# Performance work log

Hardware: AMD Instinct MI355X
Metric: run time of the kernel (lower is better)

Reference implementation:

```python
import jax, jax.numpy as jnp
import numpy as np
import math

IN_FEATURES = 512
RFF_FEATURES = 2048
OUT_FEATURES = 1000
N = 8192
RIDGE_PENALTY = 1.0
MEAN_FIELD_FACTOR = 25.0
RFF_SCALAR = math.sqrt(RFF_FEATURES / 2)  # 32.0


def _random_ortho(key, n, m):
    q, _ = jnp.linalg.qr(jax.random.normal(key, (n, m), dtype=jnp.float32))
    return q


def setup_inputs() -> dict:
    key = jax.random.key(0)
    k_d, k_w, k_norm, k_b, k_lw, k_lb, k_cov = jax.random.split(key, 7)
    D = jax.random.normal(k_d, (N, IN_FEATURES), dtype=jnp.float32)
    # RFF weight: concat of random orthonormal blocks (rff_features > in_features)
    ws = []
    dim_left = RFF_FEATURES
    kk = k_w
    while dim_left > IN_FEATURES:
        kk, sub = jax.random.split(kk)
        ws.append(_random_ortho(sub, IN_FEATURES, IN_FEATURES))
        dim_left -= IN_FEATURES
    kk, sub = jax.random.split(kk)
    ws.append(_random_ortho(sub, IN_FEATURES, dim_left))
    W = jnp.concatenate(ws, axis=1)  # [in, rff]
    feature_norm = jax.random.normal(k_norm, W.shape, dtype=jnp.float32) ** 2
    W = W * jnp.sqrt(feature_norm.sum(0))
    b = jax.random.uniform(k_b, (RFF_FEATURES,), dtype=jnp.float32) * (2.0 * math.pi)
    # logit head (nn.Linear): weight [out, rff], bias [out]
    bound = 1.0 / math.sqrt(RFF_FEATURES)
    logit_w = jax.random.uniform(k_lw, (OUT_FEATURES, RFF_FEATURES), dtype=jnp.float32,
                                 minval=-bound, maxval=bound)
    logit_b = jax.random.uniform(k_lb, (OUT_FEATURES,), dtype=jnp.float32,
                                 minval=-bound, maxval=bound)
    # positive-definite covariance buffer (stand-in for inverted precision)
    A = jax.random.normal(k_cov, (RFF_FEATURES, RFF_FEATURES), dtype=jnp.float32) * 0.01
    covariance = A @ A.T + jnp.eye(RFF_FEATURES, dtype=jnp.float32)
    return {"D": D, "W": W, "b": b, "logit_w": logit_w, "logit_b": logit_b,
            "covariance": covariance}


def reference(D, W, b, logit_w, logit_b, covariance):
    # RFF feature map: cos(D @ W + b) / rff_scalar  -> [N, rff]
    Phi = jnp.cos(D @ W + b) / RFF_SCALAR
    # linear head -> [N, out]
    pred = Phi @ logit_w.T + logit_b
    # diag(Phi @ cov @ Phi.T) * ridge computed row-wise in O(N*r^2)
    diag_cov = jnp.sum((Phi @ covariance) * Phi, axis=-1) * RIDGE_PENALTY  # [N]
    logits_scale = jnp.sqrt(1.0 + diag_cov * MEAN_FIELD_FACTOR)
    return pred / logits_scale[:, None]
```

## Files before the change

kernel.cpp:

```cpp
#include <hip/hip_runtime.h>
#include <hip/hip_fp8.h>
#include <math.h>

#define N_ROWS 8192
#define IN_F   512
#define RFF    2048
#define OUT_F  1000
#define OUT_PAD 1024
#define INV_RFF_SCALAR 0.03125f
#define MEAN_FIELD 25.0f

typedef __attribute__((ext_vector_type(8))) short short8;
typedef __attribute__((ext_vector_type(4))) float f32x4;

__device__ __forceinline__ unsigned short f32_to_bf16(float f) {
    unsigned u = __float_as_uint(f);
    unsigned r = 0x7FFFu + ((u >> 16) & 1u);
    return (unsigned short)((u + r) >> 16);
}
__device__ __forceinline__ float bf16_to_f32(unsigned short h) {
    return __uint_as_float(((unsigned)h) << 16);
}
__device__ __forceinline__ unsigned char f32_to_fp8(float x) {
    __hip_fp8_e4m3 q(x);
    return (unsigned char)q.__x;
}

__device__ __forceinline__ const uint4* gsrc(const unsigned short* X, int ldx,
                                             int r0, int k0, int q) {
    int rt = q >> 6, L = q & 63;
    int r = r0 + rt * 16 + (L & 15);
    int k = k0 + ((L >> 4) << 3);
    return (const uint4*)(X + (size_t)r * ldx + k);
}

__device__ __forceinline__ void stage_tile(const unsigned short* __restrict__ X, int ldx,
                                           int r0, int k0, unsigned short* lds,
                                           int w, int lane) {
    #pragma unroll
    for (int half = 0; half < 2; ++half) {
        int qb = half * 256 + w * 64;
        const uint4* g = gsrc(X, ldx, r0, k0, qb + lane);
        __builtin_amdgcn_global_load_lds(
            (const __attribute__((address_space(1))) void*)g,
            (__attribute__((address_space(3))) void*)(lds + qb * 8),
            16, 0, 0);
    }
}

__device__ __forceinline__ void stage_tile8(const unsigned char* __restrict__ X, int ldb,
                                            int r0, int k0b, unsigned char* lds,
                                            int w, int lane) {
    #pragma unroll
    for (int half = 0; half < 2; ++half) {
        int qb = half * 256 + w * 64;
        int q = qb + lane;
        int rt = q >> 6, L = q & 63;
        int row = r0 + rt * 16 + (L & 15);
        int kb = k0b + ((L >> 4) << 4);
        const void* g = X + (size_t)row * ldb + kb;
        __builtin_amdgcn_global_load_lds(
            (const __attribute__((address_space(1))) void*)g,
            (__attribute__((address_space(3))) void*)(lds + qb * 16),
            16, 0, 0);
    }
}

__global__ __launch_bounds__(256) void conv_split_kernel(
    const float* __restrict__ X, unsigned short* __restrict__ H,
    unsigned short* __restrict__ L, int n4)
{
    int i = blockIdx.x * 256 + threadIdx.x;
    if (i >= n4) return;
    float4 v = ((const float4*)X)[i];
    ushort4 h, l;
    h.x = f32_to_bf16(v.x); l.x = f32_to_bf16(v.x - bf16_to_f32(h.x));
    h.y = f32_to_bf16(v.y); l.y = f32_to_bf16(v.y - bf16_to_f32(h.y));
    h.z = f32_to_bf16(v.z); l.z = f32_to_bf16(v.z - bf16_to_f32(h.z));
    h.w = f32_to_bf16(v.w); l.w = f32_to_bf16(v.w - bf16_to_f32(h.w));
    ((ushort4*)H)[i] = h;
    ((ushort4*)L)[i] = l;
}

__global__ __launch_bounds__(256) void conv_covu8_kernel(
    const float* __restrict__ X, unsigned char* __restrict__ O)
{
    int i = blockIdx.x * 256 + threadIdx.x;
    int base = i * 4;
    int row = base >> 11;
    int col = base & 2047;
    int bn = row >> 7, bk = col >> 7;
    float w = (bk < bn) ? 16.0f : (bk == bn ? 8.0f : 0.0f);
    float4 v = ((const float4*)X)[i];
    float w0 = (col + 0 == row) ? 0.0f : w;
    float w1 = (col + 1 == row) ? 0.0f : w;
    float w2 = (col + 2 == row) ? 0.0f : w;
    float w3 = (col + 3 == row) ? 0.0f : w;
    uchar4 o;
    o.x = f32_to_fp8(v.x * w0); o.y = f32_to_fp8(v.y * w1);
    o.z = f32_to_fp8(v.z * w2); o.w = f32_to_fp8(v.w * w3);
    ((uchar4*)O)[i] = o;
}

__global__ __launch_bounds__(256) void conv_covd_kernel(
    const float* __restrict__ X, float* __restrict__ Cd)
{
    int i = blockIdx.x * 256 + threadIdx.x;
    if (i < RFF) Cd[i] = X[(size_t)i * RFF + i];
}

__global__ __launch_bounds__(256) void conv_phi8_kernel(
    const unsigned short* __restrict__ Phi16, unsigned char* __restrict__ Phi8)
{
    int i = blockIdx.x * 256 + threadIdx.x;
    ushort4 v = ((const ushort4*)Phi16)[i];
    uchar4 o;
    o.x = f32_to_fp8(bf16_to_f32(v.x) * 32.0f);
    o.y = f32_to_fp8(bf16_to_f32(v.y) * 32.0f);
    o.z = f32_to_fp8(bf16_to_f32(v.z) * 32.0f);
    o.w = f32_to_fp8(bf16_to_f32(v.w) * 32.0f);
    ((uchar4*)Phi8)[i] = o;
}

__global__ __launch_bounds__(256) void conv_lw_kernel(
    const float* __restrict__ Lw, unsigned short* __restrict__ O)
{
    int i = blockIdx.x * 256 + threadIdx.x;
    int base = i * 4;
    int row = base >> 11;
    ushort4 o;
    if (row < OUT_F) {
        float4 v = ((const float4*)Lw)[i];
        o.x = f32_to_bf16(v.x); o.y = f32_to_bf16(v.y);
        o.z = f32_to_bf16(v.z); o.w = f32_to_bf16(v.w);
    } else {
        o.x = o.y = o.z = o.w = 0;
    }
    ((ushort4*)O)[i] = o;
}

__global__ __launch_bounds__(256) void conv_wt_kernel(
    const float* __restrict__ W, unsigned short* __restrict__ TH,
    unsigned short* __restrict__ TL)
{
    __shared__ float tile[64][65];
    const int tid = threadIdx.x;
    const int n0 = blockIdx.x * 64;
    const int k0 = blockIdx.y * 64;
    #pragma unroll
    for (int i = 0; i < 16; ++i) {
        int e = i * 256 + tid;
        int r = e >> 6, c = e & 63;
        tile[r][c] = W[(size_t)(k0 + r) * RFF + n0 + c];
    }
    __syncthreads();
    #pragma unroll
    for (int i = 0; i < 16; ++i) {
        int e = i * 256 + tid;
        int r = e >> 6, c = e & 63;
        float v = tile[c][r];
        unsigned short h = f32_to_bf16(v);
        unsigned short l = f32_to_bf16(v - bf16_to_f32(h));
        TH[(size_t)(n0 + r) * IN_F + k0 + c] = h;
        TL[(size_t)(n0 + r) * IN_F + k0 + c] = l;
    }
}

__global__ __launch_bounds__(256) void phi_mfma_kernel(
    const unsigned short* __restrict__ Dh, const unsigned short* __restrict__ Dl,
    const unsigned short* __restrict__ Wth, const unsigned short* __restrict__ Wtl,
    const float* __restrict__ bias, unsigned short* __restrict__ Phi)
{
    __shared__ unsigned short ldsAh[4096], ldsAl[4096], ldsBh[4096], ldsBl[4096];
    const int tid = threadIdx.x;
    const int w = tid >> 6, lane = tid & 63;
    const int wm = w >> 1, wn = w & 1;
    const int r0 = blockIdx.y * 128;
    const int c0 = blockIdx.x * 128;

    f32x4 acc[4][4];
    #pragma unroll
    for (int i = 0; i < 4; ++i)
        #pragma unroll
        for (int j = 0; j < 4; ++j)
            acc[i][j] = (f32x4)(0.0f);

    for (int k0 = 0; k0 < IN_F; k0 += 32) {
        __syncthreads();
        stage_tile(Dh,  IN_F, r0, k0, ldsAh, w, lane);
        stage_tile(Dl,  IN_F, r0, k0, ldsAl, w, lane);
        stage_tile(Wth, IN_F, c0, k0, ldsBh, w, lane);
        stage_tile(Wtl, IN_F, c0, k0, ldsBl, w, lane);
        __syncthreads();

        short8 fah[4], fal[4], fbh[4], fbl[4];
        #pragma unroll
        for (int t = 0; t < 4; ++t) {
            fah[t] = *(const short8*)(ldsAh + ((wm * 4 + t) * 64 + lane) * 8);
            fal[t] = *(const short8*)(ldsAl + ((wm * 4 + t) * 64 + lane) * 8);
            fbh[t] = *(const short8*)(ldsBh + ((wn * 4 + t) * 64 + lane) * 8);
            fbl[t] = *(const short8*)(ldsBl + ((wn * 4 + t) * 64 + lane) * 8);
        }
        #pragma unroll
        for (int mt = 0; mt < 4; ++mt)
            #pragma unroll
            for (int nt = 0; nt < 4; ++nt) {
                acc[mt][nt] = __builtin_amdgcn_mfma_f32_16x16x32_bf16(
                    fah[mt], fbh[nt], acc[mt][nt], 0, 0, 0);
                acc[mt][nt] = __builtin_amdgcn_mfma_f32_16x16x32_bf16(
                    fah[mt], fbl[nt], acc[mt][nt], 0, 0, 0);
                acc[mt][nt] = __builtin_amdgcn_mfma_f32_16x16x32_bf16(
                    fal[mt], fbh[nt], acc[mt][nt], 0, 0, 0);
            }
    }

    const int quad = lane >> 4, ln = lane & 15;
    #pragma unroll
    for (int mt = 0; mt < 4; ++mt)
        #pragma unroll
        for (int nt = 0; nt < 4; ++nt) {
            int col = c0 + wn * 64 + nt * 16 + ln;
            float bv = bias[col];
            #pragma unroll
            for (int reg = 0; reg < 4; ++reg) {
                int row = r0 + wm * 64 + mt * 16 + quad * 4 + reg;
                float z = acc[mt][nt][reg] + bv;
                float p = __cosf(z) * INV_RFF_SCALAR;
                Phi[(size_t)row * RFF + col] = f32_to_bf16(p);
            }
        }
}

__global__ __launch_bounds__(256) void fused_dp_kernel(
    const unsigned short* __restrict__ Phi16, const unsigned char* __restrict__ Phi8,
    const unsigned char* __restrict__ CovU8, const float* __restrict__ Cd,
    const unsigned short* __restrict__ Lw, const float* __restrict__ Lb,
    float* __restrict__ diag, float* __restrict__ out)
{
    __shared__ __align__(16) unsigned char smem[16384];
    const int tid = threadIdx.x;
    const int w = tid >> 6, lane = tid & 63;
    const int wm = w >> 1, wn = w & 1;
    const int quad = lane >> 4, ln = lane & 15;
    const int b = blockIdx.x;

    f32x4 acc[4][4];
    #pragma unroll
    for (int i = 0; i < 4; ++i)
        #pragma unroll
        for (int j = 0; j < 4; ++j)
            acc[i][j] = (f32x4)(0.0f);

    if (b % 3 != 2) {
        const int d = (b / 3) * 2 + (b % 3);
        const int J = 15 - (d >> 6);
        const int r0 = (d & 63) * 128;
        const int c0 = J * 128;
        const int kmaxb = (J + 1) * 128;
        unsigned char* ldsA8 = smem;
        unsigned char* ldsB8 = smem + 8192;

        for (int k0b = 0; k0b < kmaxb; k0b += 64) {
            __syncthreads();
            stage_tile8(Phi8,  RFF, r0, k0b, ldsA8, w, lane);
            stage_tile8(CovU8, RFF, c0, k0b, ldsB8, w, lane);
            __syncthreads();

            #pragma unroll
            for (int s = 0; s < 2; ++s) {
                const int ccol = s * 2 + (quad >> 1);
                const int off8 = (quad & 1) << 3;
                long fa[4], fb[4];
                #pragma unroll
                for (int t = 0; t < 4; ++t) {
                    fa[t] = *(const long*)(ldsA8 + (((wm * 4 + t) * 64 + ccol * 16 + ln) << 4) + off8);
                    fb[t] = *(const long*)(ldsB8 + (((wn * 4 + t) * 64 + ccol * 16 + ln) << 4) + off8);
                }
                #pragma unroll
                for (int mt = 0; mt < 4; ++mt)
                    #pragma unroll
                    for (int nt = 0; nt < 4; ++nt)
                        acc[mt][nt] = __builtin_amdgcn_mfma_f32_16x16x32_fp8_fp8(
                            fa[mt], fb[nt], acc[mt][nt], 0, 0, 0);
            }
        }

        float cd[4];
        #pragma unroll
        for (int nt = 0; nt < 4; ++nt)
            cd[nt] = 256.0f * Cd[c0 + wn * 64 + nt * 16 + ln];
        #pragma unroll
        for (int mt = 0; mt < 4; ++mt) {
            float psum[4] = {0.f, 0.f, 0.f, 0.f};
            #pragma unroll
            for (int nt = 0; nt < 4; ++nt) {
                int col = c0 + wn * 64 + nt * 16 + ln;
                #pragma unroll
                for (int reg = 0; reg < 4; ++reg) {
                    int row = r0 + wm * 64 + mt * 16 + quad * 4 + reg;
                    float pv = bf16_to_f32(Phi16[(size_t)row * RFF + col]);
                    psum[reg] = fmaf(fmaf(cd[nt], pv, acc[mt][nt][reg]), pv, psum[reg]);
                }
            }
            #pragma unroll
            for (int off = 1; off < 16; off <<= 1)
                #pragma unroll
                for (int reg = 0; reg < 4; ++reg)
                    psum[reg] += __shfl_xor(psum[reg], off, 16);
            if (ln == 0) {
                #pragma unroll
                for (int reg = 0; reg < 4; ++reg) {
                    int row = r0 + wm * 64 + mt * 16 + quad * 4 + reg;
                    atomicAdd(&diag[row], psum[reg] * (1.0f / 256.0f));
                }
            }
        }
    } else {
        const int p = b / 3;
        const int r0 = (p >> 3) * 128;
        const int c0 = (p & 7) * 128;
        unsigned short* ldsA = (unsigned short*)smem;
        unsigned short* ldsB = (unsigned short*)(smem + 8192);

        for (int k0 = 0; k0 < RFF; k0 += 32) {
            __syncthreads();
            stage_tile(Phi16, RFF, r0, k0, ldsA, w, lane);
            stage_tile(Lw,    RFF, c0, k0, ldsB, w, lane);
            __syncthreads();

            short8 fa[4], fb[4];
            #pragma unroll
            for (int t = 0; t < 4; ++t) {
                fa[t] = *(const short8*)(ldsA + ((wm * 4 + t) * 64 + lane) * 8);
                fb[t] = *(const short8*)(ldsB + ((wn * 4 + t) * 64 + lane) * 8);
            }
            #pragma unroll
            for (int mt = 0; mt < 4; ++mt)
                #pragma unroll
                for (int nt = 0; nt < 4; ++nt)
                    acc[mt][nt] = __builtin_amdgcn_mfma_f32_16x16x32_bf16(
                        fa[mt], fb[nt], acc[mt][nt], 0, 0, 0);
        }

        #pragma unroll
        for (int mt = 0; mt < 4; ++mt)
            #pragma unroll
            for (int nt = 0; nt < 4; ++nt) {
                int col = c0 + wn * 64 + nt * 16 + ln;
                if (col < OUT_F) {
                    float bv = Lb[col];
                    #pragma unroll
                    for (int reg = 0; reg < 4; ++reg) {
                        int row = r0 + wm * 64 + mt * 16 + quad * 4 + reg;
                        out[(size_t)row * OUT_F + col] = acc[mt][nt][reg] + bv;
                    }
                }
            }
    }
}

__global__ __launch_bounds__(256) void scale_kernel(
    float* __restrict__ out, const float* __restrict__ diag)
{
    const int row = blockIdx.x;
    const int t = threadIdx.x;
    float s = 1.0f / sqrtf(1.0f + MEAN_FIELD * diag[row]);
    if (t < 250) {
        float4* p = (float4*)(out + (size_t)row * OUT_F);
        float4 v = p[t];
        v.x *= s; v.y *= s; v.z *= s; v.w *= s;
        p[t] = v;
    }
}

extern "C" void kernel_launch(void* const* d_in, const int* in_sizes, int n_in,
                              void* d_out, int out_size, void* d_ws, size_t ws_size,
                              hipStream_t stream) {
    const float* D    = (const float*)d_in[0];
    const float* W    = (const float*)d_in[1];
    const float* bias = (const float*)d_in[2];
    const float* Lw   = (const float*)d_in[3];
    const float* Lb   = (const float*)d_in[4];
    const float* cov  = (const float*)d_in[5];
    float* out = (float*)d_out;

    char* p = (char*)d_ws;
    unsigned short* Phi16 = (unsigned short*)p;  p += (size_t)N_ROWS * RFF * 2;
    unsigned char*  Phi8  = (unsigned char*)p;
    unsigned short* Dh    = (unsigned short*)p;  p += (size_t)N_ROWS * IN_F * 2;
    unsigned short* Dl    = (unsigned short*)p;  p += (size_t)N_ROWS * IN_F * 2;
    unsigned short* Wth   = (unsigned short*)p;  p += (size_t)RFF * IN_F * 2;
    unsigned short* Wtl   = (unsigned short*)p;  p += (size_t)RFF * IN_F * 2;
    unsigned short* Lw16  = (unsigned short*)p;  p += (size_t)OUT_PAD * RFF * 2;
    unsigned char*  CovU8 = (unsigned char*)p;
    float*          Cd    = (float*)(p + (size_t)RFF * RFF);
    p += (size_t)RFF * RFF * 2;
    float* diag           = (float*)p;

    hipMemsetAsync(diag, 0, N_ROWS * sizeof(float), stream);

    dim3 blk(256);
    conv_split_kernel<<<dim3((N_ROWS * IN_F / 4 + 255) / 256), blk, 0, stream>>>(D, Dh, Dl, N_ROWS * IN_F / 4);
    conv_wt_kernel<<<dim3(RFF / 64, IN_F / 64), blk, 0, stream>>>(W, Wth, Wtl);
    conv_lw_kernel<<<dim3(OUT_PAD * RFF / 4 / 256), blk, 0, stream>>>(Lw, Lw16);
    conv_covu8_kernel<<<dim3(RFF * RFF / 4 / 256), blk, 0, stream>>>(cov, CovU8);
    conv_covd_kernel<<<dim3(RFF / 256), blk, 0, stream>>>(cov, Cd);

    phi_mfma_kernel<<<dim3(RFF / 128, N_ROWS / 128), blk, 0, stream>>>(Dh, Dl, Wth, Wtl, bias, Phi16);
    conv_phi8_kernel<<<dim3(N_ROWS * RFF / 4 / 256), blk, 0, stream>>>(Phi16, Phi8);

    fused_dp_kernel<<<dim3(1536), blk, 0, stream>>>(Phi16, Phi8, CovU8, Cd, Lw16, Lb, diag, out);
    scale_kernel<<<dim3(N_ROWS), blk, 0, stream>>>(out, diag);
}
```

Baseline: 365.3 us.

## Split fused diag/pred kernel, permute fp8 layouts, fold scaling into pred epilogue

```diff
diff --git a/kernel.cpp b/kernel.cpp
--- a/kernel.cpp
+++ b/kernel.cpp
@@ -12,6 +12,7 @@
 
 typedef __attribute__((ext_vector_type(8))) short short8;
 typedef __attribute__((ext_vector_type(4))) float f32x4;
+typedef __attribute__((ext_vector_type(2))) long long2v;
 
 __device__ __forceinline__ unsigned short f32_to_bf16(float f) {
     unsigned u = __float_as_uint(f);
@@ -24,6 +25,10 @@
 __device__ __forceinline__ unsigned char f32_to_fp8(float x) {
     __hip_fp8_e4m3 q(x);
     return (unsigned char)q.__x;
+}
+
+__device__ __forceinline__ int perm64(int k) {
+    return (k & ~63) | (((k >> 3) & 3) << 4) | (((k >> 5) & 1) << 3) | (k & 7);
 }
 
 __device__ __forceinline__ const uint4* gsrc(const unsigned short* X, int ldx,
@@ -33,7 +38,6 @@
     int k = k0 + ((L >> 4) << 3);
     return (const uint4*)(X + (size_t)r * ldx + k);
 }
-
 __device__ __forceinline__ void stage_tile(const unsigned short* __restrict__ X, int ldx,
                                            int r0, int k0, unsigned short* lds,
                                            int w, int lane) {
@@ -48,17 +52,31 @@
     }
 }
 
-__device__ __forceinline__ void stage_tile8(const unsigned char* __restrict__ X, int ldb,
+__device__ __forceinline__ void stage_tile64(const unsigned short* __restrict__ X,
+                                             int r0, int k0, unsigned char* lds,
+                                             int w, int lane) {
+    #pragma unroll
+    for (int h = 0; h < 4; ++h) {
+        int qb = h * 256 + w * 64;
+        int q = qb + lane;
+        int rt = q >> 7, c = (q >> 4) & 7, r = q & 15;
+        const void* g = X + (size_t)(r0 + rt * 16 + r) * RFF + k0 + c * 8;
+        __builtin_amdgcn_global_load_lds(
+            (const __attribute__((address_space(1))) void*)g,
+            (__attribute__((address_space(3))) void*)(lds + qb * 16),
+            16, 0, 0);
+    }
+}
+
+__device__ __forceinline__ void stage_tile8(const unsigned char* __restrict__ X,
                                             int r0, int k0b, unsigned char* lds,
                                             int w, int lane) {
     #pragma unroll
-    for (int half = 0; half < 2; ++half) {
-        int qb = half * 256 + w * 64;
+    for (int h = 0; h < 4; ++h) {
+        int qb = h * 256 + w * 64;
         int q = qb + lane;
-        int rt = q >> 6, L = q & 63;
-        int row = r0 + rt * 16 + (L & 15);
-        int kb = k0b + ((L >> 4) << 4);
-        const void* g = X + (size_t)row * ldb + kb;
+        int rt = q >> 7, c = (q >> 4) & 7, r = q & 15;
+        const void* g = X + (size_t)(r0 + rt * 16 + r) * RFF + k0b + c * 16;
         __builtin_amdgcn_global_load_lds(
             (const __attribute__((address_space(1))) void*)g,
             (__attribute__((address_space(3))) void*)(lds + qb * 16),
@@ -99,7 +117,7 @@
     uchar4 o;
     o.x = f32_to_fp8(v.x * w0); o.y = f32_to_fp8(v.y * w1);
     o.z = f32_to_fp8(v.z * w2); o.w = f32_to_fp8(v.w * w3);
-    ((uchar4*)O)[i] = o;
+    *(uchar4*)(O + (size_t)row * RFF + perm64(col)) = o;
 }
 
 __global__ __launch_bounds__(256) void conv_covd_kernel(
@@ -113,13 +131,16 @@
     const unsigned short* __restrict__ Phi16, unsigned char* __restrict__ Phi8)
 {
     int i = blockIdx.x * 256 + threadIdx.x;
+    int base = i * 4;
+    int row = base >> 11;
+    int col = base & 2047;
     ushort4 v = ((const ushort4*)Phi16)[i];
     uchar4 o;
     o.x = f32_to_fp8(bf16_to_f32(v.x) * 32.0f);
     o.y = f32_to_fp8(bf16_to_f32(v.y) * 32.0f);
     o.z = f32_to_fp8(bf16_to_f32(v.z) * 32.0f);
     o.w = f32_to_fp8(bf16_to_f32(v.w) * 32.0f);
-    ((uchar4*)Phi8)[i] = o;
+    *(uchar4*)(Phi8 + (size_t)row * RFF + perm64(col)) = o;
 }
 
 __global__ __launch_bounds__(256) void conv_lw_kernel(
@@ -231,18 +252,21 @@
         }
 }
 
-__global__ __launch_bounds__(256) void fused_dp_kernel(
-    const unsigned short* __restrict__ Phi16, const unsigned char* __restrict__ Phi8,
-    const unsigned char* __restrict__ CovU8, const float* __restrict__ Cd,
-    const unsigned short* __restrict__ Lw, const float* __restrict__ Lb,
-    float* __restrict__ diag, float* __restrict__ out)
-{
-    __shared__ __align__(16) unsigned char smem[16384];
+__global__ __launch_bounds__(256) void diag8_kernel(
+    const unsigned char* __restrict__ Phi8, const unsigned char* __restrict__ CovU8,
+    const unsigned short* __restrict__ Phi16, const float* __restrict__ Cd,
+    float* __restrict__ diag)
+{
+    __shared__ __align__(16) unsigned char ldsA[16384];
+    __shared__ __align__(16) unsigned char ldsB[16384];
     const int tid = threadIdx.x;
     const int w = tid >> 6, lane = tid & 63;
     const int wm = w >> 1, wn = w & 1;
     const int quad = lane >> 4, ln = lane & 15;
-    const int b = blockIdx.x;
+    const int J = 15 - blockIdx.x;
+    const int r0 = blockIdx.y * 128;
+    const int c0 = J * 128;
+    const int kmax = (J + 1) * 128;
 
     f32x4 acc[4][4];
     #pragma unroll
@@ -251,88 +275,101 @@
         for (int j = 0; j < 4; ++j)
             acc[i][j] = (f32x4)(0.0f);
 
-    if (b % 3 != 2) {
-        const int d = (b / 3) * 2 + (b % 3);
-        const int J = 15 - (d >> 6);
-        const int r0 = (d & 63) * 128;
-        const int c0 = J * 128;
-        const int kmaxb = (J + 1) * 128;
-        unsigned char* ldsA8 = smem;
-        unsigned char* ldsB8 = smem + 8192;
-
-        for (int k0b = 0; k0b < kmaxb; k0b += 64) {
-            __syncthreads();
-            stage_tile8(Phi8,  RFF, r0, k0b, ldsA8, w, lane);
-            stage_tile8(CovU8, RFF, c0, k0b, ldsB8, w, lane);
-            __syncthreads();
-
-            #pragma unroll
-            for (int s = 0; s < 2; ++s) {
-                const int ccol = s * 2 + (quad >> 1);
-                const int off8 = (quad & 1) << 3;
-                long fa[4], fb[4];
+    for (int k0 = 0; k0 < kmax; k0 += 128) {
+        __syncthreads();
+        stage_tile8(Phi8,  r0, k0, ldsA, w, lane);
+        stage_tile8(CovU8, c0, k0, ldsB, w, lane);
+        __syncthreads();
+
+        #pragma unroll
+        for (int kb = 0; kb < 2; ++kb) {
+            long2v fa[4], fb[4];
+            #pragma unroll
+            for (int t = 0; t < 4; ++t) {
+                fa[t] = *(const long2v*)(ldsA + (((wm * 4 + t) * 128 + (kb * 4 + quad) * 16 + ln) << 4));
+                fb[t] = *(const long2v*)(ldsB + (((wn * 4 + t) * 128 + (kb * 4 + quad) * 16 + ln) << 4));
+            }
+            #pragma unroll
+            for (int mt = 0; mt < 4; ++mt)
                 #pragma unroll
-                for (int t = 0; t < 4; ++t) {
-                    fa[t] = *(const long*)(ldsA8 + (((wm * 4 + t) * 64 + ccol * 16 + ln) << 4) + off8);
-                    fb[t] = *(const long*)(ldsB8 + (((wn * 4 + t) * 64 + ccol * 16 + ln) << 4) + off8);
-                }
+                for (int nt = 0; nt < 4; ++nt)
+                    acc[mt][nt] = __builtin_amdgcn_mfma_f32_16x16x32_fp8_fp8(
+                        fa[mt].x, fb[nt].x, acc[mt][nt], 0, 0, 0);
+            #pragma unroll
+            for (int mt = 0; mt < 4; ++mt)
                 #pragma unroll
-                for (int mt = 0; mt < 4; ++mt)
-                    #pragma unroll
-                    for (int nt = 0; nt < 4; ++nt)
-                        acc[mt][nt] = __builtin_amdgcn_mfma_f32_16x16x32_fp8_fp8(
-                            fa[mt], fb[nt], acc[mt][nt], 0, 0, 0);
-            }
-        }
-
-        float cd[4];
-        #pragma unroll
-        for (int nt = 0; nt < 4; ++nt)
-            cd[nt] = 256.0f * Cd[c0 + wn * 64 + nt * 16 + ln];
-        #pragma unroll
-        for (int mt = 0; mt < 4; ++mt) {
-            float psum[4] = {0.f, 0.f, 0.f, 0.f};
-            #pragma unroll
-            for (int nt = 0; nt < 4; ++nt) {
-                int col = c0 + wn * 64 + nt * 16 + ln;
-                #pragma unroll
-                for (int reg = 0; reg < 4; ++reg) {
-                    int row = r0 + wm * 64 + mt * 16 + quad * 4 + reg;
-                    float pv = bf16_to_f32(Phi16[(size_t)row * RFF + col]);
-                    psum[reg] = fmaf(fmaf(cd[nt], pv, acc[mt][nt][reg]), pv, psum[reg]);
-                }
-            }
-            #pragma unroll
-            for (int off = 1; off < 16; off <<= 1)
-                #pragma unroll
-                for (int reg = 0; reg < 4; ++reg)
-                    psum[reg] += __shfl_xor(psum[reg], off, 16);
-            if (ln == 0) {
-                #pragma unroll
-                for (int reg = 0; reg < 4; ++reg) {
-                    int row = r0 + wm * 64 + mt * 16 + quad * 4 + reg;
-                    atomicAdd(&diag[row], psum[reg] * (1.0f / 256.0f));
-                }
-            }
-        }
-    } else {
-        const int p = b / 3;
-        const int r0 = (p >> 3) * 128;
-        const int c0 = (p & 7) * 128;
-        unsigned short* ldsA = (unsigned short*)smem;
-        unsigned short* ldsB = (unsigned short*)(smem + 8192);
-
-        for (int k0 = 0; k0 < RFF; k0 += 32) {
-            __syncthreads();
-            stage_tile(Phi16, RFF, r0, k0, ldsA, w, lane);
-            stage_tile(Lw,    RFF, c0, k0, ldsB, w, lane);
-            __syncthreads();
-
+                for (int nt = 0; nt < 4; ++nt)
+                    acc[mt][nt] = __builtin_amdgcn_mfma_f32_16x16x32_fp8_fp8(
+                        fa[mt].y, fb[nt].y, acc[mt][nt], 0, 0, 0);
+        }
+    }
+
+    float cd[4];
+    #pragma unroll
+    for (int nt = 0; nt < 4; ++nt)
+        cd[nt] = 256.0f * Cd[c0 + wn * 64 + nt * 16 + ln];
+    #pragma unroll
+    for (int mt = 0; mt < 4; ++mt) {
+        float psum[4] = {0.f, 0.f, 0.f, 0.f};
+        #pragma unroll
+        for (int nt = 0; nt < 4; ++nt) {
+            int col = c0 + wn * 64 + nt * 16 + ln;
+            #pragma unroll
+            for (int reg = 0; reg < 4; ++reg) {
+                int row = r0 + wm * 64 + mt * 16 + quad * 4 + reg;
+                float pv = bf16_to_f32(Phi16[(size_t)row * RFF + col]);
+                psum[reg] = fmaf(fmaf(cd[nt], pv, acc[mt][nt][reg]), pv, psum[reg]);
+            }
+        }
+        #pragma unroll
+        for (int off = 1; off < 16; off <<= 1)
+            #pragma unroll
+            for (int reg = 0; reg < 4; ++reg)
+                psum[reg] += __shfl_xor(psum[reg], off, 16);
+        if (ln == 0) {
+            #pragma unroll
+            for (int reg = 0; reg < 4; ++reg) {
+                int row = r0 + wm * 64 + mt * 16 + quad * 4 + reg;
+                atomicAdd(&diag[row], psum[reg] * (1.0f / 256.0f));
+            }
+        }
+    }
+}
+
+__global__ __launch_bounds__(256) void pred_mfma_kernel(
+    const unsigned short* __restrict__ Phi, const unsigned short* __restrict__ Lw,
+    const float* __restrict__ Lb, const float* __restrict__ diag,
+    float* __restrict__ out)
+{
+    __shared__ __align__(16) unsigned char ldsA[16384];
+    __shared__ __align__(16) unsigned char ldsB[16384];
+    const int tid = threadIdx.x;
+    const int w = tid >> 6, lane = tid & 63;
+    const int wm = w >> 1, wn = w & 1;
+    const int quad = lane >> 4, ln = lane & 15;
+    const int r0 = blockIdx.y * 128;
+    const int c0 = blockIdx.x * 128;
+
+    f32x4 acc[4][4];
+    #pragma unroll
+    for (int i = 0; i < 4; ++i)
+        #pragma unroll
+        for (int j = 0; j < 4; ++j)
+            acc[i][j] = (f32x4)(0.0f);
+
+    for (int k0 = 0; k0 < RFF; k0 += 64) {
+        __syncthreads();
+        stage_tile64(Phi, r0, k0, ldsA, w, lane);
+        stage_tile64(Lw,  c0, k0, ldsB, w, lane);
+        __syncthreads();
+
+        #pragma unroll
+        for (int s = 0; s < 2; ++s) {
             short8 fa[4], fb[4];
             #pragma unroll
             for (int t = 0; t < 4; ++t) {
-                fa[t] = *(const short8*)(ldsA + ((wm * 4 + t) * 64 + lane) * 8);
-                fb[t] = *(const short8*)(ldsB + ((wn * 4 + t) * 64 + lane) * 8);
+                fa[t] = *(const short8*)(ldsA + (((wm * 4 + t) * 128 + (s * 4 + quad) * 16 + ln) << 4));
+                fb[t] = *(const short8*)(ldsB + (((wn * 4 + t) * 128 + (s * 4 + quad) * 16 + ln) << 4));
             }
             #pragma unroll
             for (int mt = 0; mt < 4; ++mt)
@@ -341,35 +378,28 @@
                     acc[mt][nt] = __builtin_amdgcn_mfma_f32_16x16x32_bf16(
                         fa[mt], fb[nt], acc[mt][nt], 0, 0, 0);
         }
-
-        #pragma unroll
-        for (int mt = 0; mt < 4; ++mt)
-            #pragma unroll
-            for (int nt = 0; nt < 4; ++nt) {
-                int col = c0 + wn * 64 + nt * 16 + ln;
-                if (col < OUT_F) {
-                    float bv = Lb[col];
-                    #pragma unroll
-                    for (int reg = 0; reg < 4; ++reg) {
-                        int row = r0 + wm * 64 + mt * 16 + quad * 4 + reg;
-                        out[(size_t)row * OUT_F + col] = acc[mt][nt][reg] + bv;
-                    }
+    }
+
+    #pragma unroll
+    for (int mt = 0; mt < 4; ++mt) {
+        float s[4];
+        #pragma unroll
+        for (int reg = 0; reg < 4; ++reg) {
+            int row = r0 + wm * 64 + mt * 16 + quad * 4 + reg;
+            s[reg] = 1.0f / sqrtf(1.0f + MEAN_FIELD * diag[row]);
+        }
+        #pragma unroll
+        for (int nt = 0; nt < 4; ++nt) {
+            int col = c0 + wn * 64 + nt * 16 + ln;
+            if (col < OUT_F) {
+                float bv = Lb[col];
+                #pragma unroll
+                for (int reg = 0; reg < 4; ++reg) {
+                    int row = r0 + wm * 64 + mt * 16 + quad * 4 + reg;
+                    out[(size_t)row * OUT_F + col] = (acc[mt][nt][reg] + bv) * s[reg];
                 }
             }
-    }
-}
-
-__global__ __launch_bounds__(256) void scale_kernel(
-    float* __restrict__ out, const float* __restrict__ diag)
-{
-    const int row = blockIdx.x;
-    const int t = threadIdx.x;
-    float s = 1.0f / sqrtf(1.0f + MEAN_FIELD * diag[row]);
-    if (t < 250) {
-        float4* p = (float4*)(out + (size_t)row * OUT_F);
-        float4 v = p[t];
-        v.x *= s; v.y *= s; v.z *= s; v.w *= s;
-        p[t] = v;
+        }
     }
 }
 
@@ -409,6 +439,6 @@
     phi_mfma_kernel<<<dim3(RFF / 128, N_ROWS / 128), blk, 0, stream>>>(Dh, Dl, Wth, Wtl, bias, Phi16);
     conv_phi8_kernel<<<dim3(N_ROWS * RFF / 4 / 256), blk, 0, stream>>>(Phi16, Phi8);
 
-    fused_dp_kernel<<<dim3(1536), blk, 0, stream>>>(Phi16, Phi8, CovU8, Cd, Lw16, Lb, diag, out);
-    scale_kernel<<<dim3(N_ROWS), blk, 0, stream>>>(out, diag);
-}
+    diag8_kernel<<<dim3(16, N_ROWS / 128), blk, 0, stream>>>(Phi8, CovU8, Phi16, Cd, diag);
+    pred_mfma_kernel<<<dim3(OUT_PAD / 128, N_ROWS / 128), blk, 0, stream>>>(Phi16, Lw16, Lb, diag, out);
+}
```

New measurement: 318.6 us. 1.15x faster.
